# Kernel optimization log

Measured on AMD Instinct MI355X. Metric: run time of the kernel, lower is better.

The kernel has to match this reference:

```python
import jax, jax.numpy as jnp
import numpy as np

VN, BN, NSW, EC, MN = 64, 200, 10, 63, 73
FIN, HID = 32, 64
VLOW, VUPP = 0.9, 1.1


def _ln(z, eps=1e-5):
    m = jnp.mean(z, axis=-1, keepdims=True)
    v = jnp.var(z, axis=-1, keepdims=True)
    return (z - m) * jax.lax.rsqrt(v + eps)


def _layer(x, s, conn, deg_inv, Ws, Wi, Wj, U, Vw, first):
    # dense gated edge update over (B,V,V,H)
    e = jnp.einsum('bvwh,hk->bvwk', s, Ws) + (x @ Wi)[:, :, None, :] + (x @ Wj)[:, None, :, :]
    e = jax.nn.relu(_ln(e))
    s_out = e if first else s + e
    gate = jax.nn.sigmoid(s_out) * conn[None, :, :, None]
    msg = jnp.einsum('bvwh,bwh->bvh', gate, x @ Vw) * deg_inv[None, :, None]  # mean agg
    h = jax.nn.relu(_ln(x @ U + msg))
    return (h if first else x + h), s_out


def setup_inputs() -> dict:
    key = jax.random.key(0)
    ks = jax.random.split(key, 24)
    # radial feeder: path graph (line edges) + long-range tie switches, i<j (triu)
    ea = np.stack([np.arange(VN - 1), np.arange(1, VN)]).astype(np.int32)
    es = np.stack([np.arange(NSW), np.arange(NSW) + 32]).astype(np.int32)
    A = np.zeros((VN, VN), np.float32); A[ea[0], ea[1]] = 1; A[ea[1], ea[0]] = 1
    S = np.zeros((VN, VN), np.float32); S[es[0], es[1]] = 1; S[es[1], es[0]] = 1
    par = np.concatenate([ea[0], es[0]]); chi = np.concatenate([ea[1], es[1]])
    Incp = np.zeros((VN, MN), np.float32); Incp[par, np.arange(MN)] = 1
    Incc = np.zeros((VN, MN), np.float32); Incc[chi, np.arange(MN)] = 1
    deg = (A + S).sum(1)
    Dinv = np.diag((1.0 / np.maximum(deg, 1.0)).astype(np.float32))

    def w(k, shape):
        return jax.random.normal(k, shape, jnp.float32) / np.sqrt(shape[-2])

    return {
        'x': jax.random.normal(ks[0], (BN, VN, FIN), jnp.float32),
        'A': jnp.asarray(A), 'S': jnp.asarray(S),
        'embed_s': jax.random.normal(ks[1], (2, FIN), jnp.float32),
        'p0_Ws': w(ks[2], (FIN, HID)), 'p0_Wi': w(ks[3], (FIN, HID)),
        'p0_Wj': w(ks[4], (FIN, HID)), 'p0_U': w(ks[5], (FIN, HID)),
        'p0_V': w(ks[6], (FIN, HID)),
        'pl_Ws': w(ks[7], (2, HID, HID)), 'pl_Wi': w(ks[8], (2, HID, HID)),
        'pl_Wj': w(ks[9], (2, HID, HID)), 'pl_U': w(ks[10], (2, HID, HID)),
        'pl_V': w(ks[11], (2, HID, HID)),
        'smlp_W1': w(ks[12], (4 * HID, 4 * HID)), 'smlp_W2': w(ks[13], (4 * HID, 4)),
        'cmlp_W1': w(ks[14], (3 * HID, 3 * HID)), 'cmlp_W2': w(ks[15], (3 * HID, 3)),
        'Dinv': jnp.asarray(Dinv), 'Incp': jnp.asarray(Incp), 'Incc': jnp.asarray(Incc),
        'edge_A': jnp.asarray(ea), 'edge_S': jnp.asarray(es),
    }


def reference(x, A, S, embed_s, p0_Ws, p0_Wi, p0_Wj, p0_U, p0_V,
              pl_Ws, pl_Wi, pl_Wj, pl_U, pl_V,
              smlp_W1, smlp_W2, cmlp_W1, cmlp_W2,
              Dinv, Incp, Incc, edge_A, edge_S):
    B = x.shape[0]
    conn = jnp.clip(A + S, 0.0, 1.0)                       # (V,V) union adjacency
    deg_inv = 1.0 / jnp.maximum(conn.sum(1), 1.0)
    # init_embed_edges over dense S -> (B,V,V,FIN)
    s = jnp.broadcast_to(embed_s[S.astype(jnp.int32)][None], (B, VN, VN, FIN))
    xh, s = _layer(x, s, conn, deg_inv, p0_Ws, p0_Wi, p0_Wj, p0_U, p0_V, True)
    for l in range(pl_Ws.shape[0]):
        xh, s = _layer(xh, s, conn, deg_inv, pl_Ws[l], pl_Wi[l], pl_Wj[l], pl_U[l], pl_V[l], False)
    x_g = xh.sum(1)                                        # (B,H) graph feature

    # -- switch head (gather at triu switch edges, identical across batch) --
    si, sj = edge_S[0], edge_S[1]
    xg_s = jnp.broadcast_to(x_g[:, None, :], (B, si.shape[0], HID))
    smlp_in = jnp.concatenate([s[:, si, sj, :], xh[:, si], xh[:, sj], xg_s], axis=-1)
    smlp_out = jax.nn.sigmoid(jax.nn.relu(smlp_in @ smlp_W1) @ smlp_W2)  # (B,nsw,4)
    topology = smlp_out[..., 0]
    graph_topo = jnp.concatenate([jnp.ones((B, MN - NSW), x.dtype), topology], axis=1)
    ps = smlp_out[..., 1] - 0.5
    vs_p = VLOW * (1 - smlp_out[..., 2]) + VUPP * smlp_out[..., 2]
    vs_c = VLOW * (1 - smlp_out[..., 3]) + VUPP * smlp_out[..., 3]

    # -- connection head (gather at triu line edges) --
    ai, aj = edge_A[0], edge_A[1]
    xg_c = jnp.broadcast_to(x_g[:, None, :], (B, ai.shape[0], HID))
    cmlp_in = jnp.concatenate([xh[:, ai], xh[:, aj], xg_c], axis=-1)
    cmlp_out = jax.nn.sigmoid(jax.nn.relu(cmlp_in @ cmlp_W1) @ cmlp_W2)  # (B,Ec,3)
    pc = cmlp_out[..., 0] - 0.5
    vc_p = VLOW * (1 - cmlp_out[..., 1]) + VUPP * cmlp_out[..., 1]
    vc_c = VLOW * (1 - cmlp_out[..., 2]) + VUPP * cmlp_out[..., 2]

    # scatter into (B,M) physics tensors: first M-nsw cols from CMLP, last nsw from SMLP
    p_flow = jnp.concatenate([pc, ps], axis=1)
    v_par = jnp.concatenate([vc_p, vs_p], axis=1)
    v_chi = jnp.concatenate([vc_c, vs_c], axis=1)
    v = v_par @ (Dinv @ Incp).T + v_chi @ (Dinv @ Incc).T   # (B,V)
    v = v.at[:, 0].set(1.0)
    return jnp.concatenate([p_flow, v, graph_topo], axis=1)  # (B, M+V+M)
```

## Files before the change

### kernel.cpp

```cpp
#include <hip/hip_runtime.h>

#define BN 200
#define VN 64
#define HIDD 64
#define FINN 32
#define NSW 10
#define EC 63
#define MNE 73
#define NEDGE 146
#define NPACK 128

typedef unsigned short u16;
typedef unsigned int u32;
typedef __attribute__((ext_vector_type(8))) short bf16x8;
typedef __attribute__((ext_vector_type(4))) float f32x4;

__device__ __forceinline__ float bfu(u16 u) { return __uint_as_float(((u32)u) << 16); }
__device__ __forceinline__ u16 f2bf(float f) {
    u32 x = __float_as_uint(f);
    u32 r = x + 0x7fffu + ((x >> 16) & 1u);
    return (u16)(r >> 16);
}
__device__ __forceinline__ float cvtv(const void* p, int i, int fl) {
    return fl ? bfu(((const u16*)p)[i]) : ((const float*)p)[i];
}

__device__ __forceinline__ int swz(int row, int col) { return col ^ ((row & 7) << 3); }

__device__ __forceinline__ float ldp(const u16* H, const u16* L, int idx) {
    return bfu(H[idx]) + bfu(L[idx]);
}
__device__ __forceinline__ void stp(u16* H, u16* L, int idx, float f) {
    u16 h = f2bf(f);
    H[idx] = h;
    L[idx] = f2bf(f - bfu(h));
}

__device__ __forceinline__ void ln2(float ea, float eb, float& ra, float& rb) {
    float a1 = ea, a2 = ea * ea, b1 = eb, b2 = eb * eb;
#pragma unroll
    for (int m = 1; m < 64; m <<= 1) {
        a1 += __shfl_xor(a1, m);
        a2 += __shfl_xor(a2, m);
        b1 += __shfl_xor(b1, m);
        b2 += __shfl_xor(b2, m);
    }
    float ma = a1 * 0.015625f, mb = b1 * 0.015625f;
    float va = fmaxf(a2 * 0.015625f - ma * ma, 0.f);
    float vb = fmaxf(b2 * 0.015625f - mb * mb, 0.f);
    ra = fmaxf((ea - ma) * rsqrtf(va + 1e-5f), 0.f);
    rb = fmaxf((eb - mb) * rsqrtf(vb + 1e-5f), 0.f);
}

__device__ __forceinline__ void ln4(float ea, float eb, float ec, float ed,
                                    float& ra, float& rb, float& rc, float& rd) {
    float a1 = ea, a2 = ea * ea, b1 = eb, b2 = eb * eb;
    float c1 = ec, c2 = ec * ec, d1 = ed, d2 = ed * ed;
#pragma unroll
    for (int m = 1; m < 64; m <<= 1) {
        a1 += __shfl_xor(a1, m); a2 += __shfl_xor(a2, m);
        b1 += __shfl_xor(b1, m); b2 += __shfl_xor(b2, m);
        c1 += __shfl_xor(c1, m); c2 += __shfl_xor(c2, m);
        d1 += __shfl_xor(d1, m); d2 += __shfl_xor(d2, m);
    }
    float ma = a1 * 0.015625f, mb = b1 * 0.015625f;
    float mc = c1 * 0.015625f, md = d1 * 0.015625f;
    float va = fmaxf(a2 * 0.015625f - ma * ma, 0.f);
    float vb = fmaxf(b2 * 0.015625f - mb * mb, 0.f);
    float vc = fmaxf(c2 * 0.015625f - mc * mc, 0.f);
    float vd = fmaxf(d2 * 0.015625f - md * md, 0.f);
    ra = fmaxf((ea - ma) * rsqrtf(va + 1e-5f), 0.f);
    rb = fmaxf((eb - mb) * rsqrtf(vb + 1e-5f), 0.f);
    rc = fmaxf((ec - mc) * rsqrtf(vc + 1e-5f), 0.f);
    rd = fmaxf((ed - md) * rsqrtf(vd + 1e-5f), 0.f);
}

struct CvtArgs { const void* src[21]; };

__global__ __launch_bounds__(256) void k_prep(CvtArgs ca, const int* __restrict__ eA,
                                              const int* __restrict__ eS,
                                              u16* __restrict__ c1h, u16* __restrict__ c1l,
                                              u16* __restrict__ c2h, u16* __restrict__ c2l,
                                              u16* __restrict__ s1h, u16* __restrict__ s1l,
                                              u16* __restrict__ s2h, u16* __restrict__ s2l,
                                              u16* __restrict__ w0h, u16* __restrict__ w0l,
                                              u16* __restrict__ wlh, u16* __restrict__ wll,
                                              float* __restrict__ ews, float* __restrict__ dinv,
                                              int* __restrict__ row_ptr, int* __restrict__ colp,
                                              int* __restrict__ sw_eidx,
                                              float* __restrict__ dinvD, int* __restrict__ incCnt,
                                              int* __restrict__ incM) {
    int t = threadIdx.x;
    int fl = (((const u16*)ca.src[1])[1] == 0x3F80) ? 1 : 0;
    if (blockIdx.x == 0) {
        __shared__ unsigned char flagL[64 * 65];
        __shared__ float wsL[FINN * 64];
        __shared__ float emL[64];
        __shared__ int degL[64], rpS[65], colS[NEDGE + 16];
        __shared__ int eAL[2 * EC], eSL[2 * NSW];

        if (t < 2 * EC) eAL[t] = eA[t];
        if (t >= 128 && t < 128 + 2 * NSW) eSL[t - 128] = eS[t - 128];
        if (t >= 160 && t < 224) emL[t - 160] = cvtv(ca.src[3], t - 160, fl);
        for (int i = t; i < FINN * 64; i += 256) wsL[i] = cvtv(ca.src[4], i, fl);
        for (int i = t; i < 4096; i += 256) {
            float a = cvtv(ca.src[1], i, fl);
            float s = cvtv(ca.src[2], i, fl);
            int r = i >> 6, c = i & 63;
            flagL[r * 65 + c] = (unsigned char)(((a != 0.f || s != 0.f) ? 1 : 0) |
                                                ((s != 0.f) ? 2 : 0));
        }
        __syncthreads();

        if (t < 128) {
            int j = t >> 6, k = t & 63;
            float a = 0.f;
#pragma unroll
            for (int h = 0; h < FINN; h++) a += emL[j * FINN + h] * wsL[h * 64 + k];
            ews[(j << 6) + k] = a;
        }
        if (t < 64) {
            int d = 0;
#pragma unroll
            for (int w = 0; w < 64; w++) d += flagL[t * 65 + w] & 1;
            degL[t] = d;
            dinv[t] = 1.f / fmaxf((float)d, 1.f);
        }
        __syncthreads();
        if (t == 0) {
            int c = 0;
            for (int v = 0; v < 64; v++) { rpS[v] = c; c += degL[v]; }
            rpS[64] = c;
        }
        __syncthreads();
        if (t < 65) row_ptr[t] = rpS[t];
        if (t < 64) {
            int pos = rpS[t];
#pragma unroll
            for (int w = 0; w < 64; w++) {
                int f = flagL[t * 65 + w];
                if (f & 1) colS[pos++] = w | ((f & 2) ? 256 : 0) | (t << 16);
            }
        }
        __syncthreads();
        int tot = rpS[64];
        if (t < tot) colp[t] = colS[t];
        if (t < NSW) {
            int si = eSL[t], sj = eSL[NSW + t];
            int idx = 0;
            for (int e = rpS[si]; e < rpS[si + 1]; e++)
                if ((colS[e] & 255) == sj) idx = e;
            sw_eidx[t] = idx;
        }
        if (t < 64) {
            dinvD[t] = cvtv(ca.src[18], t * 64 + t, fl);
            int cnt = 0;
            for (int m = 0; m < MNE; m++) {
                int par = (m < EC) ? eAL[m] : eSL[m - EC];
                int chi = (m < EC) ? eAL[EC + m] : eSL[NSW + (m - EC)];
                if (par == t && cnt < 8) incM[t * 8 + cnt++] = (m << 1);
                if (chi == t && cnt < 8) incM[t * 8 + cnt++] = (m << 1) | 1;
            }
            incCnt[t] = cnt;
        }
    } else {
        const int T1 = 36864, T2 = T1 + 3072, T3 = T2 + 65536, T4 = T3 + 4096;
        const int T5 = T4 + 8192, TOT = T5 + 40960;
        for (int i = (blockIdx.x - 1) * 256 + t; i < TOT; i += NPACK * 256) {
            int idx = i;
            const void* src;
            u16 *dh, *dl;
            int K2, N2, nt, rem, loff = 0;
            if (idx < T1) {
                nt = idx / 3072; rem = idx - nt * 3072; src = ca.src[16];
                dh = c1h + idx; dl = c1l + idx; K2 = 192; N2 = 192;
            } else if (idx < T2) {
                idx -= T1; nt = 0; rem = idx; src = ca.src[17];
                dh = c2h + idx; dl = c2l + idx; K2 = 192; N2 = 3;
            } else if (idx < T3) {
                idx -= T2; nt = idx >> 12; rem = idx & 4095; src = ca.src[14];
                dh = s1h + idx; dl = s1l + idx; K2 = 256; N2 = 256;
            } else if (idx < T4) {
                idx -= T3; nt = 0; rem = idx; src = ca.src[15];
                dh = s2h + idx; dl = s2l + idx; K2 = 256; N2 = 4;
            } else if (idx < T5) {
                int j = idx - T4;
                int mt = j >> 11;
                int m2 = j & 2047;
                nt = m2 >> 9; rem = m2 & 511; src = ca.src[5 + mt];
                dh = w0h + j; dl = w0l + j; K2 = 32; N2 = 64;
            } else {
                int j = idx - T5;
                int l = j / 20480;
                int jj = j - l * 20480;
                int mt = jj >> 12;
                int m2 = jj & 4095;
                nt = m2 >> 10; rem = m2 & 1023; src = ca.src[9 + mt];
                loff = l * 4096;
                dh = wlh + j; dl = wll + j; K2 = 64; N2 = 64;
            }
            int kb = rem >> 9, r8 = rem & 511, ln = r8 >> 3, jq = r8 & 7;
            int k = kb * 32 + ((ln >> 4) << 3) + jq;
            int n = nt * 16 + (ln & 15);
            float val = 0.f;
            if (n < N2 && k < K2) val = cvtv(src, loff + k * N2 + n, fl);
            u16 h = f2bf(val);
            *dh = h;
            *dl = f2bf(val - bfu(h));
        }
    }
}

#define XI 0
#define XJ 1
#define XU 2
#define XV 3

__global__ __launch_bounds__(1024) void k_main(
    const void* __restrict__ xraw, const u16* __restrict__ A_u16,
    const int* __restrict__ eA, const int* __restrict__ eS,
    const float* __restrict__ ews, const float* __restrict__ dinv,
    const int* __restrict__ row_ptr, const int* __restrict__ colp,
    const int* __restrict__ sw_eidx,
    const float* __restrict__ dinvD, const int* __restrict__ incCnt, const int* __restrict__ incM,
    const u16* __restrict__ w0h, const u16* __restrict__ w0l,
    const u16* __restrict__ wlh, const u16* __restrict__ wll,
    const u16* __restrict__ c1h, const u16* __restrict__ c1l,
    const u16* __restrict__ c2h, const u16* __restrict__ c2l,
    const u16* __restrict__ s1h, const u16* __restrict__ s1l,
    const u16* __restrict__ s2h, const u16* __restrict__ s2l,
    void* __restrict__ out_v)
{
    __shared__ __align__(16) u16 xHp[64 * 64], xLp[64 * 64];
    __shared__ __align__(16) u16 sHp[NEDGE * 64], sLp[NEDGE * 64];
    __shared__ __align__(16) float preL[NEDGE * 64];
    __shared__ __align__(16) float tLs[4 * 64 * 64];
    __shared__ __align__(16) u16 xgH[64], xgLo[64];
    __shared__ float ewsL[128];
    __shared__ float dinvL[64];
    __shared__ int rpL[65];
    __shared__ int colL[NEDGE + 6];
    __shared__ int swLx[NSW];
    __shared__ int eALs[2 * EC], eSLs[2 * NSW];
    __shared__ float cmoL[EC * 3], smoL[NSW * 4];

    int b = blockIdx.x, t = threadIdx.x;
    int lane = t & 63, wid = t >> 6;
    int m = lane & 15, quad = lane >> 4;
    int fl = (A_u16[1] == 0x3F80) ? 1 : 0;

    for (int i = t; i < 2048; i += 1024) {
        int r = i >> 5, c = i & 31;
        stp(xHp, xLp, (r << 6) + swz(r, c), cvtv(xraw, b * 2048 + i, fl));
    }
    if (t < 128) ewsL[t] = ews[t];
    if (t < 64) dinvL[t] = dinv[t];
    if (t < 65) rpL[t] = row_ptr[t];
    if (t < NEDGE) colL[t] = colp[t];
    if (t < NSW) swLx[t] = sw_eidx[t];
    if (t >= 256 && t < 256 + 2 * EC) eALs[t - 256] = eA[t - 256];
    if (t >= 512 && t < 512 + 2 * NSW) eSLs[t - 512] = eS[t - 512];
    __syncthreads();

    {
        int mat = wid >> 2, Mt = wid & 3;
        const u16* bhp = w0h + mat * 2048;
        const u16* blp = w0l + mat * 2048;
        int row = Mt * 16 + m;
        int c0 = quad * 8;
        bf16x8 ah = *(const bf16x8*)&xHp[(row << 6) + swz(row, c0)];
        bf16x8 al = *(const bf16x8*)&xLp[(row << 6) + swz(row, c0)];
        f32x4 acc[4];
#pragma unroll
        for (int nt = 0; nt < 4; nt++) acc[nt] = (f32x4){0.f, 0.f, 0.f, 0.f};
#pragma unroll
        for (int nt = 0; nt < 4; nt++) {
            int o = (nt << 9) + (lane << 3);
            bf16x8 bh = *(const bf16x8*)(bhp + o);
            bf16x8 bl = *(const bf16x8*)(blp + o);
            acc[nt] = __builtin_amdgcn_mfma_f32_16x16x32_bf16(ah, bh, acc[nt], 0, 0, 0);
            acc[nt] = __builtin_amdgcn_mfma_f32_16x16x32_bf16(al, bh, acc[nt], 0, 0, 0);
            acc[nt] = __builtin_amdgcn_mfma_f32_16x16x32_bf16(ah, bl, acc[nt], 0, 0, 0);
        }
#pragma unroll
        for (int nt = 0; nt < 4; nt++)
#pragma unroll
            for (int r = 0; r < 4; r++) {
                int orow = Mt * 16 + quad * 4 + r;
                tLs[mat * 4096 + (orow << 6) + swz(orow, nt * 16 + m)] = acc[nt][r];
            }
    }
    __syncthreads();

    for (int e = wid; e < NEDGE; e += 32) {
        int e2i = e + 16;
        int has2 = (e2i < NEDGE);
        int eb2 = has2 ? e2i : e;
        int cpa = colL[e], cpb = colL[eb2];
        int wa = cpa & 255, va = (cpa >> 16) & 255;
        int wb = cpb & 255, vb = (cpb >> 16) & 255;
        int sia = (e << 6) + swz(e, lane);
        int sib = (eb2 << 6) + swz(eb2, lane);
        float eea = ewsL[(((cpa >> 8) & 1) << 6) + lane]
                  + tLs[XI * 4096 + (va << 6) + swz(va, lane)]
                  + tLs[XJ * 4096 + (wa << 6) + swz(wa, lane)];
        float eeb = ewsL[(((cpb >> 8) & 1) << 6) + lane]
                  + tLs[XI * 4096 + (vb << 6) + swz(vb, lane)]
                  + tLs[XJ * 4096 + (wb << 6) + swz(wb, lane)];
        float ha, hb;
        ln2(eea, eeb, ha, hb);
        stp(sHp, sLp, sia, ha);
        preL[sia] = tLs[XV * 4096 + (wa << 6) + swz(wa, lane)]
                  * __fdividef(1.f, 1.f + __expf(-ha));
        if (has2) {
            stp(sHp, sLp, sib, hb);
            preL[sib] = tLs[XV * 4096 + (wb << 6) + swz(wb, lane)]
                      * __fdividef(1.f, 1.f + __expf(-hb));
        }
    }
    __syncthreads();

    {
        int v0 = wid << 2;
        float mc0 = 0.f, mc1 = 0.f, mc2 = 0.f, mc3 = 0.f;
        for (int e = rpL[v0]; e < rpL[v0 + 1]; e++) mc0 += preL[(e << 6) + swz(e, lane)];
        for (int e = rpL[v0 + 1]; e < rpL[v0 + 2]; e++) mc1 += preL[(e << 6) + swz(e, lane)];
        for (int e = rpL[v0 + 2]; e < rpL[v0 + 3]; e++) mc2 += preL[(e << 6) + swz(e, lane)];
        for (int e = rpL[v0 + 3]; e < rpL[v0 + 4]; e++) mc3 += preL[(e << 6) + swz(e, lane)];
        float z0 = tLs[XU * 4096 + ((v0 + 0) << 6) + swz(v0 + 0, lane)] + mc0 * dinvL[v0 + 0];
        float z1 = tLs[XU * 4096 + ((v0 + 1) << 6) + swz(v0 + 1, lane)] + mc1 * dinvL[v0 + 1];
        float z2 = tLs[XU * 4096 + ((v0 + 2) << 6) + swz(v0 + 2, lane)] + mc2 * dinvL[v0 + 2];
        float z3 = tLs[XU * 4096 + ((v0 + 3) << 6) + swz(v0 + 3, lane)] + mc3 * dinvL[v0 + 3];
        float h0, h1, h2, h3;
        ln4(z0, z1, z2, z3, h0, h1, h2, h3);
        stp(xHp, xLp, ((v0 + 0) << 6) + swz(v0 + 0, lane), h0);
        stp(xHp, xLp, ((v0 + 1) << 6) + swz(v0 + 1, lane), h1);
        stp(xHp, xLp, ((v0 + 2) << 6) + swz(v0 + 2, lane), h2);
        stp(xHp, xLp, ((v0 + 3) << 6) + swz(v0 + 3, lane), h3);
    }
    __syncthreads();

    for (int l = 0; l < 2; l++) {
        {
            int mat = wid >> 2, Mt = wid & 3;
            const u16* bhp = wlh + l * 20480 + (mat + 1) * 4096;
            const u16* blp = wll + l * 20480 + (mat + 1) * 4096;
            int row = Mt * 16 + m;
            f32x4 acc[4];
#pragma unroll
            for (int nt = 0; nt < 4; nt++) acc[nt] = (f32x4){0.f, 0.f, 0.f, 0.f};
#pragma unroll
            for (int kb = 0; kb < 2; kb++) {
                int c0 = kb * 32 + quad * 8;
                bf16x8 ah = *(const bf16x8*)&xHp[(row << 6) + swz(row, c0)];
                bf16x8 al = *(const bf16x8*)&xLp[(row << 6) + swz(row, c0)];
#pragma unroll
                for (int nt = 0; nt < 4; nt++) {
                    int o = (((nt << 1) + kb) << 9) + (lane << 3);
                    bf16x8 bh = *(const bf16x8*)(bhp + o);
                    bf16x8 bl = *(const bf16x8*)(blp + o);
                    acc[nt] = __builtin_amdgcn_mfma_f32_16x16x32_bf16(ah, bh, acc[nt], 0, 0, 0);
                    acc[nt] = __builtin_amdgcn_mfma_f32_16x16x32_bf16(al, bh, acc[nt], 0, 0, 0);
                    acc[nt] = __builtin_amdgcn_mfma_f32_16x16x32_bf16(ah, bl, acc[nt], 0, 0, 0);
                }
            }
#pragma unroll
            for (int nt = 0; nt < 4; nt++)
#pragma unroll
                for (int r = 0; r < 4; r++) {
                    int orow = Mt * 16 + quad * 4 + r;
                    tLs[mat * 4096 + (orow << 6) + swz(orow, nt * 16 + m)] = acc[nt][r];
                }

            const u16* sbh = wlh + l * 20480;
            const u16* sbl = wll + l * 20480;
            for (int u = wid; u < 40; u += 16) {
                int rt = u >> 2, ntq = u & 3;
                int srow = rt * 16 + m;
                int ar = (srow > NEDGE - 1) ? (NEDGE - 1) : srow;
                f32x4 sacc = (f32x4){0.f, 0.f, 0.f, 0.f};
#pragma unroll
                for (int kb = 0; kb < 2; kb++) {
                    int c0 = kb * 32 + quad * 8;
                    bf16x8 ah = *(const bf16x8*)&sHp[(ar << 6) + swz(ar, c0)];
                    bf16x8 al = *(const bf16x8*)&sLp[(ar << 6) + swz(ar, c0)];
                    int o = (((ntq << 1) + kb) << 9) + (lane << 3);
                    bf16x8 bh = *(const bf16x8*)(sbh + o);
                    bf16x8 bl = *(const bf16x8*)(sbl + o);
                    sacc = __builtin_amdgcn_mfma_f32_16x16x32_bf16(ah, bh, sacc, 0, 0, 0);
                    sacc = __builtin_amdgcn_mfma_f32_16x16x32_bf16(al, bh, sacc, 0, 0, 0);
                    sacc = __builtin_amdgcn_mfma_f32_16x16x32_bf16(ah, bl, sacc, 0, 0, 0);
                }
#pragma unroll
                for (int r = 0; r < 4; r++) {
                    int orow = rt * 16 + quad * 4 + r;
                    if (orow < NEDGE)
                        preL[(orow << 6) + swz(orow, ntq * 16 + m)] = sacc[r];
                }
            }
        }
        __syncthreads();

        for (int e = wid; e < NEDGE; e += 32) {
            int e2i = e + 16;
            int has2 = (e2i < NEDGE);
            int eb2 = has2 ? e2i : e;
            int cpa = colL[e], cpb = colL[eb2];
            int wa = cpa & 255, va = (cpa >> 16) & 255;
            int wb = cpb & 255, vb = (cpb >> 16) & 255;
            int sia = (e << 6) + swz(e, lane);
            int sib = (eb2 << 6) + swz(eb2, lane);
            float eea = preL[sia]
                      + tLs[XI * 4096 + (va << 6) + swz(va, lane)]
                      + tLs[XJ * 4096 + (wa << 6) + swz(wa, lane)];
            float eeb = preL[sib]
                      + tLs[XI * 4096 + (vb << 6) + swz(vb, lane)]
                      + tLs[XJ * 4096 + (wb << 6) + swz(wb, lane)];
            float ha, hb;
            ln2(eea, eeb, ha, hb);
            float souta = ldp(sHp, sLp, sia) + ha;
            float soutb = ldp(sHp, sLp, sib) + hb;
            stp(sHp, sLp, sia, souta);
            preL[sia] = tLs[XV * 4096 + (wa << 6) + swz(wa, lane)]
                      * __fdividef(1.f, 1.f + __expf(-souta));
            if (has2) {
                stp(sHp, sLp, sib, soutb);
                preL[sib] = tLs[XV * 4096 + (wb << 6) + swz(wb, lane)]
                          * __fdividef(1.f, 1.f + __expf(-soutb));
            }
        }
        __syncthreads();

        {
            int v0 = wid << 2;
            float mc0 = 0.f, mc1 = 0.f, mc2 = 0.f, mc3 = 0.f;
            for (int e = rpL[v0]; e < rpL[v0 + 1]; e++) mc0 += preL[(e << 6) + swz(e, lane)];
            for (int e = rpL[v0 + 1]; e < rpL[v0 + 2]; e++) mc1 += preL[(e << 6) + swz(e, lane)];
            for (int e = rpL[v0 + 2]; e < rpL[v0 + 3]; e++) mc2 += preL[(e << 6) + swz(e, lane)];
            for (int e = rpL[v0 + 3]; e < rpL[v0 + 4]; e++) mc3 += preL[(e << 6) + swz(e, lane)];
            float z0 = tLs[XU * 4096 + ((v0 + 0) << 6) + swz(v0 + 0, lane)] + mc0 * dinvL[v0 + 0];
            float z1 = tLs[XU * 4096 + ((v0 + 1) << 6) + swz(v0 + 1, lane)] + mc1 * dinvL[v0 + 1];
            float z2 = tLs[XU * 4096 + ((v0 + 2) << 6) + swz(v0 + 2, lane)] + mc2 * dinvL[v0 + 2];
            float z3 = tLs[XU * 4096 + ((v0 + 3) << 6) + swz(v0 + 3, lane)] + mc3 * dinvL[v0 + 3];
            float h0, h1, h2, h3;
            ln4(z0, z1, z2, z3, h0, h1, h2, h3);
            int i0 = ((v0 + 0) << 6) + swz(v0 + 0, lane);
            int i1 = ((v0 + 1) << 6) + swz(v0 + 1, lane);
            int i2 = ((v0 + 2) << 6) + swz(v0 + 2, lane);
            int i3 = ((v0 + 3) << 6) + swz(v0 + 3, lane);
            float x0 = ldp(xHp, xLp, i0) + h0;
            float x1 = ldp(xHp, xLp, i1) + h1;
            float x2 = ldp(xHp, xLp, i2) + h2;
            float x3 = ldp(xHp, xLp, i3) + h3;
            stp(xHp, xLp, i0, x0);
            stp(xHp, xLp, i1, x1);
            stp(xHp, xLp, i2, x2);
            stp(xHp, xLp, i3, x3);
            if (l == 1) tLs[(wid << 6) + lane] = x0 + x1 + x2 + x3;
        }
        __syncthreads();
    }

    if (t < 64) {
        float s = 0.f;
#pragma unroll
        for (int i = 0; i < 16; i++) s += tLs[(i << 6) + t];
        stp(xgH, xgLo, t, s);
    }
    __syncthreads();

    u16* tp  = (u16*)tLs;
    u16* hcH = tp;
    u16* hcL = tp + 12288;
    u16* hsH = tp + 24576;
    u16* hsL = tp + 28672;

    if (wid < 12) {
        int Mt = wid & 3, ntg = wid >> 2;
        int e = Mt * 16 + m; if (e > 62) e = 62;
        int ai = eALs[e], aj = eALs[EC + e];
        f32x4 acc[4];
#pragma unroll
        for (int j = 0; j < 4; j++) acc[j] = (f32x4){0.f, 0.f, 0.f, 0.f};
#pragma unroll
        for (int kb = 0; kb < 6; kb++) {
            int k = kb * 32 + quad * 8;
            bf16x8 ah, al;
            if (k < 64) {
                ah = *(const bf16x8*)&xHp[(ai << 6) + swz(ai, k)];
                al = *(const bf16x8*)&xLp[(ai << 6) + swz(ai, k)];
            } else if (k < 128) {
                int c = k - 64;
                ah = *(const bf16x8*)&xHp[(aj << 6) + swz(aj, c)];
                al = *(const bf16x8*)&xLp[(aj << 6) + swz(aj, c)];
            } else {
                int c = k - 128;
                ah = *(const bf16x8*)&xgH[c];
                al = *(const bf16x8*)&xgLo[c];
            }
#pragma unroll
            for (int j = 0; j < 4; j++) {
                int nt = ntg * 4 + j;
                int o = ((nt * 6 + kb) << 9) + (lane << 3);
                bf16x8 bh = *(const bf16x8*)(c1h + o);
                bf16x8 bl = *(const bf16x8*)(c1l + o);
                acc[j] = __builtin_amdgcn_mfma_f32_16x16x32_bf16(ah, bh, acc[j], 0, 0, 0);
                acc[j] = __builtin_amdgcn_mfma_f32_16x16x32_bf16(al, bh, acc[j], 0, 0, 0);
                acc[j] = __builtin_amdgcn_mfma_f32_16x16x32_bf16(ah, bl, acc[j], 0, 0, 0);
            }
        }
#pragma unroll
        for (int j = 0; j < 4; j++) {
            int nt = ntg * 4 + j;
#pragma unroll
            for (int r = 0; r < 4; r++) {
                int row = Mt * 16 + quad * 4 + r;
                stp(hcH, hcL, row * 192 + swz(row, nt * 16 + m), fmaxf(acc[j][r], 0.f));
            }
        }
    } else {
        int e2 = (m > 9) ? 9 : m;
        int si = eSLs[e2], sj = eSLs[NSW + e2];
        int sw = swLx[e2];
#pragma unroll
        for (int j = 0; j < 4; j++) {
            int nt = (wid - 12) * 4 + j;
            f32x4 accS = (f32x4){0.f, 0.f, 0.f, 0.f};
#pragma unroll
            for (int kb = 0; kb < 8; kb++) {
                int k = kb * 32 + quad * 8;
                bf16x8 ah, al;
                if (k < 64) {
                    ah = *(const bf16x8*)&sHp[(sw << 6) + swz(sw, k)];
                    al = *(const bf16x8*)&sLp[(sw << 6) + swz(sw, k)];
                } else if (k < 128) {
                    int c = k - 64;
                    ah = *(const bf16x8*)&xHp[(si << 6) + swz(si, c)];
                    al = *(const bf16x8*)&xLp[(si << 6) + swz(si, c)];
                } else if (k < 192) {
                    int c = k - 128;
                    ah = *(const bf16x8*)&xHp[(sj << 6) + swz(sj, c)];
                    al = *(const bf16x8*)&xLp[(sj << 6) + swz(sj, c)];
                } else {
                    int c = k - 192;
                    ah = *(const bf16x8*)&xgH[c];
                    al = *(const bf16x8*)&xgLo[c];
                }
                int o = ((nt * 8 + kb) << 9) + (lane << 3);
                bf16x8 bh = *(const bf16x8*)(s1h + o);
                bf16x8 bl = *(const bf16x8*)(s1l + o);
                accS = __builtin_amdgcn_mfma_f32_16x16x32_bf16(ah, bh, accS, 0, 0, 0);
                accS = __builtin_amdgcn_mfma_f32_16x16x32_bf16(al, bh, accS, 0, 0, 0);
                accS = __builtin_amdgcn_mfma_f32_16x16x32_bf16(ah, bl, accS, 0, 0, 0);
            }
#pragma unroll
            for (int r = 0; r < 4; r++) {
                int row = quad * 4 + r;
                stp(hsH, hsL, (row << 8) + swz(row, nt * 16 + m), fmaxf(accS[r], 0.f));
            }
        }
    }
    __syncthreads();

    if (wid < 4) {
        f32x4 accD = (f32x4){0.f, 0.f, 0.f, 0.f};
        int row = wid * 16 + m;
#pragma unroll
        for (int kb = 0; kb < 6; kb++) {
            int c0 = kb * 32 + quad * 8;
            bf16x8 ah = *(const bf16x8*)&hcH[row * 192 + swz(row, c0)];
            bf16x8 al = *(const bf16x8*)&hcL[row * 192 + swz(row, c0)];
            int o = (kb << 9) + (lane << 3);
            bf16x8 bh = *(const bf16x8*)(c2h + o);
            bf16x8 bl = *(const bf16x8*)(c2l + o);
            accD = __builtin_amdgcn_mfma_f32_16x16x32_bf16(ah, bh, accD, 0, 0, 0);
            accD = __builtin_amdgcn_mfma_f32_16x16x32_bf16(al, bh, accD, 0, 0, 0);
            accD = __builtin_amdgcn_mfma_f32_16x16x32_bf16(ah, bl, accD, 0, 0, 0);
        }
#pragma unroll
        for (int r = 0; r < 4; r++) {
            int row2 = wid * 16 + quad * 4 + r;
            if (row2 < EC && m < 3)
                cmoL[row2 * 3 + m] = 1.f / (1.f + __expf(-accD[r]));
        }
    } else if (wid == 4) {
        f32x4 accT = (f32x4){0.f, 0.f, 0.f, 0.f};
#pragma unroll
        for (int kb = 0; kb < 8; kb++) {
            int c0 = kb * 32 + quad * 8;
            bf16x8 ah = *(const bf16x8*)&hsH[(m << 8) + swz(m, c0)];
            bf16x8 al = *(const bf16x8*)&hsL[(m << 8) + swz(m, c0)];
            int o = (kb << 9) + (lane << 3);
            bf16x8 bh = *(const bf16x8*)(s2h + o);
            bf16x8 bl = *(const bf16x8*)(s2l + o);
            accT = __builtin_amdgcn_mfma_f32_16x16x32_bf16(ah, bh, accT, 0, 0, 0);
            accT = __builtin_amdgcn_mfma_f32_16x16x32_bf16(al, bh, accT, 0, 0, 0);
            accT = __builtin_amdgcn_mfma_f32_16x16x32_bf16(ah, bl, accT, 0, 0, 0);
        }
#pragma unroll
        for (int r = 0; r < 4; r++) {
            int row = quad * 4 + r;
            if (row < NSW && m < 4)
                smoL[row * 4 + m] = 1.f / (1.f + __expf(-accT[r]));
        }
    }
    __syncthreads();

    if (t < 2 * MNE + VN) {
        float val;
        if (t < MNE) {
            val = (t < EC) ? cmoL[t * 3] - 0.5f : smoL[(t - EC) * 4 + 1] - 0.5f;
        } else if (t < MNE + VN) {
            int i = t - MNE;
            if (i == 0) {
                val = 1.0f;
            } else {
                float acc = 0.f;
                int c = incCnt[i];
                for (int q = 0; q < c; q++) {
                    int em = incM[i * 8 + q];
                    int mm = em >> 1, role = em & 1;
                    float vv = (mm < EC) ? 0.9f + 0.2f * cmoL[mm * 3 + 1 + role]
                                         : 0.9f + 0.2f * smoL[(mm - EC) * 4 + 2 + role];
                    acc += vv;
                }
                val = acc * dinvD[i];
            }
        } else {
            int mm = t - (MNE + VN);
            val = (mm < EC) ? 1.0f : smoL[(mm - EC) * 4];
        }
        size_t oidx = (size_t)b * (2 * MNE + VN) + t;
        if (fl) ((u16*)out_v)[oidx] = f2bf(val);
        else    ((float*)out_v)[oidx] = val;
    }
}

extern "C" void kernel_launch(void* const* d_in, const int* in_sizes, int n_in,
                              void* d_out, int out_size, void* d_ws, size_t ws_size,
                              hipStream_t stream) {
    const int* eA = (const int*)d_in[21];
    const int* eS = (const int*)d_in[22];

    float* pool = (float*)d_ws;
    float* ews     = pool;
    float* dinv    = ews + 128;
    float* dinvD   = dinv + 64;
    int*   row_ptr = (int*)(dinvD + 64);
    int*   colp    = row_ptr + 80;
    int*   sw_eidx = colp + 256;
    int*   incCnt  = sw_eidx + 16;
    int*   incM    = incCnt + 64;
    u16*   c1h = (u16*)(incM + 512);
    u16*   c1l = c1h + 36864;
    u16*   c2h = c1l + 36864;
    u16*   c2l = c2h + 3072;
    u16*   s1h = c2l + 3072;
    u16*   s1l = s1h + 65536;
    u16*   s2h = s1l + 65536;
    u16*   s2l = s2h + 4096;
    u16*   w0h = s2l + 4096;
    u16*   w0l = w0h + 8192;
    u16*   wlh = w0l + 8192;
    u16*   wll = wlh + 40960;

    CvtArgs ca;
    for (int i = 0; i < 21; i++) ca.src[i] = d_in[i];

    k_prep<<<1 + NPACK, 256, 0, stream>>>(ca, eA, eS,
                                          c1h, c1l, c2h, c2l, s1h, s1l, s2h, s2l,
                                          w0h, w0l, wlh, wll,
                                          ews, dinv, row_ptr, colp, sw_eidx,
                                          dinvD, incCnt, incM);

    k_main<<<BN, 1024, 0, stream>>>(d_in[0], (const u16*)d_in[1], eA, eS,
                                    ews, dinv, row_ptr, colp, sw_eidx,
                                    dinvD, incCnt, incM,
                                    w0h, w0l, wlh, wll,
                                    c1h, c1l, c2h, c2l, s1h, s1l, s2h, s2l,
                                    d_out);
}
```

Before: 179.7 us.

## Pack hi/lo bf16 pairs into u32 LDS words, use DPP layer-norm reductions

Interleaves the high and low bf16 halves of each split-precision value into one 32-bit LDS word, so scalar loads and stores touch one array and the MFMA fragments are rebuilt from two 128-bit loads with bit shuffles. The swizzle is changed to match the new word granularity. Layer-norm reductions switch from xor-shuffle butterflies to DPP row operations plus readlane. The switch-head GEMM loop is reordered so each A fragment is loaded once and reused across four output tiles. This trades fewer LDS transactions and shuffles for extra ALU unpacking work and higher register pressure.

```diff
diff --git a/kernel.cpp b/kernel.cpp
--- a/kernel.cpp
+++ b/kernel.cpp
@@ -14,6 +14,7 @@
 typedef unsigned int u32;
 typedef __attribute__((ext_vector_type(8))) short bf16x8;
 typedef __attribute__((ext_vector_type(4))) float f32x4;
+typedef __attribute__((ext_vector_type(4))) u32 u32x4;
 
 __device__ __forceinline__ float bfu(u16 u) { return __uint_as_float(((u32)u) << 16); }
 __device__ __forceinline__ u16 f2bf(float f) {
@@ -25,54 +26,54 @@
     return fl ? bfu(((const u16*)p)[i]) : ((const float*)p)[i];
 }
 
-__device__ __forceinline__ int swz(int row, int col) { return col ^ ((row & 7) << 3); }
-
-__device__ __forceinline__ float ldp(const u16* H, const u16* L, int idx) {
-    return bfu(H[idx]) + bfu(L[idx]);
-}
-__device__ __forceinline__ void stp(u16* H, u16* L, int idx, float f) {
+__device__ __forceinline__ int swzp(int row, int col) { return col ^ ((row & 7) << 2); }
+
+__device__ __forceinline__ float ldp1(const u32* P, int idx) {
+    u32 v = P[idx];
+    return __uint_as_float(v << 16) + __uint_as_float(v & 0xffff0000u);
+}
+__device__ __forceinline__ void stp1(u32* P, int idx, float f) {
     u16 h = f2bf(f);
-    H[idx] = h;
-    L[idx] = f2bf(f - bfu(h));
-}
-
-__device__ __forceinline__ void ln2(float ea, float eb, float& ra, float& rb) {
-    float a1 = ea, a2 = ea * ea, b1 = eb, b2 = eb * eb;
-#pragma unroll
-    for (int m = 1; m < 64; m <<= 1) {
-        a1 += __shfl_xor(a1, m);
-        a2 += __shfl_xor(a2, m);
-        b1 += __shfl_xor(b1, m);
-        b2 += __shfl_xor(b2, m);
-    }
-    float ma = a1 * 0.015625f, mb = b1 * 0.015625f;
-    float va = fmaxf(a2 * 0.015625f - ma * ma, 0.f);
-    float vb = fmaxf(b2 * 0.015625f - mb * mb, 0.f);
-    ra = fmaxf((ea - ma) * rsqrtf(va + 1e-5f), 0.f);
-    rb = fmaxf((eb - mb) * rsqrtf(vb + 1e-5f), 0.f);
-}
-
-__device__ __forceinline__ void ln4(float ea, float eb, float ec, float ed,
-                                    float& ra, float& rb, float& rc, float& rd) {
-    float a1 = ea, a2 = ea * ea, b1 = eb, b2 = eb * eb;
-    float c1 = ec, c2 = ec * ec, d1 = ed, d2 = ed * ed;
-#pragma unroll
-    for (int m = 1; m < 64; m <<= 1) {
-        a1 += __shfl_xor(a1, m); a2 += __shfl_xor(a2, m);
-        b1 += __shfl_xor(b1, m); b2 += __shfl_xor(b2, m);
-        c1 += __shfl_xor(c1, m); c2 += __shfl_xor(c2, m);
-        d1 += __shfl_xor(d1, m); d2 += __shfl_xor(d2, m);
-    }
-    float ma = a1 * 0.015625f, mb = b1 * 0.015625f;
-    float mc = c1 * 0.015625f, md = d1 * 0.015625f;
-    float va = fmaxf(a2 * 0.015625f - ma * ma, 0.f);
-    float vb = fmaxf(b2 * 0.015625f - mb * mb, 0.f);
-    float vc = fmaxf(c2 * 0.015625f - mc * mc, 0.f);
-    float vd = fmaxf(d2 * 0.015625f - md * md, 0.f);
-    ra = fmaxf((ea - ma) * rsqrtf(va + 1e-5f), 0.f);
-    rb = fmaxf((eb - mb) * rsqrtf(vb + 1e-5f), 0.f);
-    rc = fmaxf((ec - mc) * rsqrtf(vc + 1e-5f), 0.f);
-    rd = fmaxf((ed - md) * rsqrtf(vd + 1e-5f), 0.f);
+    u16 l = f2bf(f - bfu(h));
+    P[idx] = (u32)h | ((u32)l << 16);
+}
+
+__device__ __forceinline__ void ldfrag(const u32* P, int i0, int i1, bf16x8* ah, bf16x8* al) {
+    u32x4 w0 = *(const u32x4*)&P[i0];
+    u32x4 w1 = *(const u32x4*)&P[i1];
+    union { bf16x8 v; u32 w[4]; } A, L;
+    A.w[0] = (w0.x & 0xffffu) | (w0.y << 16);
+    A.w[1] = (w0.z & 0xffffu) | (w0.w << 16);
+    A.w[2] = (w1.x & 0xffffu) | (w1.y << 16);
+    A.w[3] = (w1.z & 0xffffu) | (w1.w << 16);
+    L.w[0] = (w0.x >> 16) | (w0.y & 0xffff0000u);
+    L.w[1] = (w0.z >> 16) | (w0.w & 0xffff0000u);
+    L.w[2] = (w1.x >> 16) | (w1.y & 0xffff0000u);
+    L.w[3] = (w1.z >> 16) | (w1.w & 0xffff0000u);
+    *ah = A.v;
+    *al = L.v;
+}
+
+template <int CTRL>
+__device__ __forceinline__ float dppadd(float x) {
+    int v = __builtin_amdgcn_update_dpp(0, __float_as_int(x), CTRL, 0xf, 0xf, 1);
+    return x + __int_as_float(v);
+}
+__device__ __forceinline__ float wtot64(float x) {
+    x = dppadd<0x111>(x);
+    x = dppadd<0x112>(x);
+    x = dppadd<0x114>(x);
+    x = dppadd<0x118>(x);
+    x = dppadd<0x142>(x);
+    x = dppadd<0x143>(x);
+    return __int_as_float(__builtin_amdgcn_readlane(__float_as_int(x), 63));
+}
+__device__ __forceinline__ float ln_dpp(float e) {
+    float s1 = wtot64(e);
+    float s2 = wtot64(e * e);
+    float mean = s1 * 0.015625f;
+    float var = fmaxf(s2 * 0.015625f - mean * mean, 0.f);
+    return fmaxf((e - mean) * rsqrtf(var + 1e-5f), 0.f);
 }
 
 struct CvtArgs { const void* src[21]; };
@@ -231,11 +232,11 @@
     const u16* __restrict__ s2h, const u16* __restrict__ s2l,
     void* __restrict__ out_v)
 {
-    __shared__ __align__(16) u16 xHp[64 * 64], xLp[64 * 64];
-    __shared__ __align__(16) u16 sHp[NEDGE * 64], sLp[NEDGE * 64];
+    __shared__ __align__(16) u32 xP[64 * 64];
+    __shared__ __align__(16) u32 sP[NEDGE * 64];
     __shared__ __align__(16) float preL[NEDGE * 64];
     __shared__ __align__(16) float tLs[4 * 64 * 64];
-    __shared__ __align__(16) u16 xgH[64], xgLo[64];
+    __shared__ __align__(16) u32 xgPk[64];
     __shared__ float ewsL[128];
     __shared__ float dinvL[64];
     __shared__ int rpL[65];
@@ -251,7 +252,7 @@
 
     for (int i = t; i < 2048; i += 1024) {
         int r = i >> 5, c = i & 31;
-        stp(xHp, xLp, (r << 6) + swz(r, c), cvtv(xraw, b * 2048 + i, fl));
+        stp1(xP, (r << 6) + swzp(r, c), cvtv(xraw, b * 2048 + i, fl));
     }
     if (t < 128) ewsL[t] = ews[t];
     if (t < 64) dinvL[t] = dinv[t];
@@ -268,8 +269,8 @@
         const u16* blp = w0l + mat * 2048;
         int row = Mt * 16 + m;
         int c0 = quad * 8;
-        bf16x8 ah = *(const bf16x8*)&xHp[(row << 6) + swz(row, c0)];
-        bf16x8 al = *(const bf16x8*)&xLp[(row << 6) + swz(row, c0)];
+        bf16x8 ah, al;
+        ldfrag(xP, (row << 6) + swzp(row, c0), (row << 6) + swzp(row, c0 + 4), &ah, &al);
         f32x4 acc[4];
 #pragma unroll
         for (int nt = 0; nt < 4; nt++) acc[nt] = (f32x4){0.f, 0.f, 0.f, 0.f};
@@ -287,7 +288,7 @@
 #pragma unroll
             for (int r = 0; r < 4; r++) {
                 int orow = Mt * 16 + quad * 4 + r;
-                tLs[mat * 4096 + (orow << 6) + swz(orow, nt * 16 + m)] = acc[nt][r];
+                tLs[mat * 4096 + (orow << 6) + swzp(orow, nt * 16 + m)] = acc[nt][r];
             }
     }
     __syncthreads();
@@ -299,22 +300,22 @@
         int cpa = colL[e], cpb = colL[eb2];
         int wa = cpa & 255, va = (cpa >> 16) & 255;
         int wb = cpb & 255, vb = (cpb >> 16) & 255;
-        int sia = (e << 6) + swz(e, lane);
-        int sib = (eb2 << 6) + swz(eb2, lane);
+        int sia = (e << 6) + swzp(e, lane);
+        int sib = (eb2 << 6) + swzp(eb2, lane);
         float eea = ewsL[(((cpa >> 8) & 1) << 6) + lane]
-                  + tLs[XI * 4096 + (va << 6) + swz(va, lane)]
-                  + tLs[XJ * 4096 + (wa << 6) + swz(wa, lane)];
+                  + tLs[XI * 4096 + (va << 6) + swzp(va, lane)]
+                  + tLs[XJ * 4096 + (wa << 6) + swzp(wa, lane)];
         float eeb = ewsL[(((cpb >> 8) & 1) << 6) + lane]
-                  + tLs[XI * 4096 + (vb << 6) + swz(vb, lane)]
-                  + tLs[XJ * 4096 + (wb << 6) + swz(wb, lane)];
-        float ha, hb;
-        ln2(eea, eeb, ha, hb);
-        stp(sHp, sLp, sia, ha);
-        preL[sia] = tLs[XV * 4096 + (wa << 6) + swz(wa, lane)]
+                  + tLs[XI * 4096 + (vb << 6) + swzp(vb, lane)]
+                  + tLs[XJ * 4096 + (wb << 6) + swzp(wb, lane)];
+        float ha = ln_dpp(eea);
+        float hb = ln_dpp(eeb);
+        stp1(sP, sia, ha);
+        preL[sia] = tLs[XV * 4096 + (wa << 6) + swzp(wa, lane)]
                   * __fdividef(1.f, 1.f + __expf(-ha));
         if (has2) {
-            stp(sHp, sLp, sib, hb);
-            preL[sib] = tLs[XV * 4096 + (wb << 6) + swz(wb, lane)]
+            stp1(sP, sib, hb);
+            preL[sib] = tLs[XV * 4096 + (wb << 6) + swzp(wb, lane)]
                       * __fdividef(1.f, 1.f + __expf(-hb));
         }
     }
@@ -323,20 +324,19 @@
     {
         int v0 = wid << 2;
         float mc0 = 0.f, mc1 = 0.f, mc2 = 0.f, mc3 = 0.f;
-        for (int e = rpL[v0]; e < rpL[v0 + 1]; e++) mc0 += preL[(e << 6) + swz(e, lane)];
-        for (int e = rpL[v0 + 1]; e < rpL[v0 + 2]; e++) mc1 += preL[(e << 6) + swz(e, lane)];
-        for (int e = rpL[v0 + 2]; e < rpL[v0 + 3]; e++) mc2 += preL[(e << 6) + swz(e, lane)];
-        for (int e = rpL[v0 + 3]; e < rpL[v0 + 4]; e++) mc3 += preL[(e << 6) + swz(e, lane)];
-        float z0 = tLs[XU * 4096 + ((v0 + 0) << 6) + swz(v0 + 0, lane)] + mc0 * dinvL[v0 + 0];
-        float z1 = tLs[XU * 4096 + ((v0 + 1) << 6) + swz(v0 + 1, lane)] + mc1 * dinvL[v0 + 1];
-        float z2 = tLs[XU * 4096 + ((v0 + 2) << 6) + swz(v0 + 2, lane)] + mc2 * dinvL[v0 + 2];
-        float z3 = tLs[XU * 4096 + ((v0 + 3) << 6) + swz(v0 + 3, lane)] + mc3 * dinvL[v0 + 3];
-        float h0, h1, h2, h3;
-        ln4(z0, z1, z2, z3, h0, h1, h2, h3);
-        stp(xHp, xLp, ((v0 + 0) << 6) + swz(v0 + 0, lane), h0);
-        stp(xHp, xLp, ((v0 + 1) << 6) + swz(v0 + 1, lane), h1);
-        stp(xHp, xLp, ((v0 + 2) << 6) + swz(v0 + 2, lane), h2);
-        stp(xHp, xLp, ((v0 + 3) << 6) + swz(v0 + 3, lane), h3);
+        for (int e = rpL[v0]; e < rpL[v0 + 1]; e++) mc0 += preL[(e << 6) + swzp(e, lane)];
+        for (int e = rpL[v0 + 1]; e < rpL[v0 + 2]; e++) mc1 += preL[(e << 6) + swzp(e, lane)];
+        for (int e = rpL[v0 + 2]; e < rpL[v0 + 3]; e++) mc2 += preL[(e << 6) + swzp(e, lane)];
+        for (int e = rpL[v0 + 3]; e < rpL[v0 + 4]; e++) mc3 += preL[(e << 6) + swzp(e, lane)];
+        float z0 = tLs[XU * 4096 + ((v0 + 0) << 6) + swzp(v0 + 0, lane)] + mc0 * dinvL[v0 + 0];
+        float z1 = tLs[XU * 4096 + ((v0 + 1) << 6) + swzp(v0 + 1, lane)] + mc1 * dinvL[v0 + 1];
+        float z2 = tLs[XU * 4096 + ((v0 + 2) << 6) + swzp(v0 + 2, lane)] + mc2 * dinvL[v0 + 2];
+        float z3 = tLs[XU * 4096 + ((v0 + 3) << 6) + swzp(v0 + 3, lane)] + mc3 * dinvL[v0 + 3];
+        float h0 = ln_dpp(z0), h1 = ln_dpp(z1), h2 = ln_dpp(z2), h3 = ln_dpp(z3);
+        stp1(xP, ((v0 + 0) << 6) + swzp(v0 + 0, lane), h0);
+        stp1(xP, ((v0 + 1) << 6) + swzp(v0 + 1, lane), h1);
+        stp1(xP, ((v0 + 2) << 6) + swzp(v0 + 2, lane), h2);
+        stp1(xP, ((v0 + 3) << 6) + swzp(v0 + 3, lane), h3);
     }
     __syncthreads();
 
@@ -352,8 +352,8 @@
 #pragma unroll
             for (int kb = 0; kb < 2; kb++) {
                 int c0 = kb * 32 + quad * 8;
-                bf16x8 ah = *(const bf16x8*)&xHp[(row << 6) + swz(row, c0)];
-                bf16x8 al = *(const bf16x8*)&xLp[(row << 6) + swz(row, c0)];
+                bf16x8 ah, al;
+                ldfrag(xP, (row << 6) + swzp(row, c0), (row << 6) + swzp(row, c0 + 4), &ah, &al);
 #pragma unroll
                 for (int nt = 0; nt < 4; nt++) {
                     int o = (((nt << 1) + kb) << 9) + (lane << 3);
@@ -369,7 +369,7 @@
 #pragma unroll
                 for (int r = 0; r < 4; r++) {
                     int orow = Mt * 16 + quad * 4 + r;
-                    tLs[mat * 4096 + (orow << 6) + swz(orow, nt * 16 + m)] = acc[nt][r];
+                    tLs[mat * 4096 + (orow << 6) + swzp(orow, nt * 16 + m)] = acc[nt][r];
                 }
 
             const u16* sbh = wlh + l * 20480;
@@ -382,8 +382,8 @@
 #pragma unroll
                 for (int kb = 0; kb < 2; kb++) {
                     int c0 = kb * 32 + quad * 8;
-                    bf16x8 ah = *(const bf16x8*)&sHp[(ar << 6) + swz(ar, c0)];
-                    bf16x8 al = *(const bf16x8*)&sLp[(ar << 6) + swz(ar, c0)];
+                    bf16x8 ah, al;
+                    ldfrag(sP, (ar << 6) + swzp(ar, c0), (ar << 6) + swzp(ar, c0 + 4), &ah, &al);
                     int o = (((ntq << 1) + kb) << 9) + (lane << 3);
                     bf16x8 bh = *(const bf16x8*)(sbh + o);
                     bf16x8 bl = *(const bf16x8*)(sbl + o);
@@ -395,7 +395,7 @@
                 for (int r = 0; r < 4; r++) {
                     int orow = rt * 16 + quad * 4 + r;
                     if (orow < NEDGE)
-                        preL[(orow << 6) + swz(orow, ntq * 16 + m)] = sacc[r];
+                        preL[(orow << 6) + swzp(orow, ntq * 16 + m)] = sacc[r];
                 }
             }
         }
@@ -408,24 +408,24 @@
             int cpa = colL[e], cpb = colL[eb2];
             int wa = cpa & 255, va = (cpa >> 16) & 255;
             int wb = cpb & 255, vb = (cpb >> 16) & 255;
-            int sia = (e << 6) + swz(e, lane);
-            int sib = (eb2 << 6) + swz(eb2, lane);
+            int sia = (e << 6) + swzp(e, lane);
+            int sib = (eb2 << 6) + swzp(eb2, lane);
             float eea = preL[sia]
-                      + tLs[XI * 4096 + (va << 6) + swz(va, lane)]
-                      + tLs[XJ * 4096 + (wa << 6) + swz(wa, lane)];
+                      + tLs[XI * 4096 + (va << 6) + swzp(va, lane)]
+                      + tLs[XJ * 4096 + (wa << 6) + swzp(wa, lane)];
             float eeb = preL[sib]
-                      + tLs[XI * 4096 + (vb << 6) + swz(vb, lane)]
-                      + tLs[XJ * 4096 + (wb << 6) + swz(wb, lane)];
-            float ha, hb;
-            ln2(eea, eeb, ha, hb);
-            float souta = ldp(sHp, sLp, sia) + ha;
-            float soutb = ldp(sHp, sLp, sib) + hb;
-            stp(sHp, sLp, sia, souta);
-            preL[sia] = tLs[XV * 4096 + (wa << 6) + swz(wa, lane)]
+                      + tLs[XI * 4096 + (vb << 6) + swzp(vb, lane)]
+                      + tLs[XJ * 4096 + (wb << 6) + swzp(wb, lane)];
+            float ha = ln_dpp(eea);
+            float hb = ln_dpp(eeb);
+            float souta = ldp1(sP, sia) + ha;
+            float soutb = ldp1(sP, sib) + hb;
+            stp1(sP, sia, souta);
+            preL[sia] = tLs[XV * 4096 + (wa << 6) + swzp(wa, lane)]
                       * __fdividef(1.f, 1.f + __expf(-souta));
             if (has2) {
-                stp(sHp, sLp, sib, soutb);
-                preL[sib] = tLs[XV * 4096 + (wb << 6) + swz(wb, lane)]
+                stp1(sP, sib, soutb);
+                preL[sib] = tLs[XV * 4096 + (wb << 6) + swzp(wb, lane)]
                           * __fdividef(1.f, 1.f + __expf(-soutb));
             }
         }
@@ -434,28 +434,27 @@
         {
             int v0 = wid << 2;
             float mc0 = 0.f, mc1 = 0.f, mc2 = 0.f, mc3 = 0.f;
-            for (int e = rpL[v0]; e < rpL[v0 + 1]; e++) mc0 += preL[(e << 6) + swz(e, lane)];
-            for (int e = rpL[v0 + 1]; e < rpL[v0 + 2]; e++) mc1 += preL[(e << 6) + swz(e, lane)];
-            for (int e = rpL[v0 + 2]; e < rpL[v0 + 3]; e++) mc2 += preL[(e << 6) + swz(e, lane)];
-            for (int e = rpL[v0 + 3]; e < rpL[v0 + 4]; e++) mc3 += preL[(e << 6) + swz(e, lane)];
-            float z0 = tLs[XU * 4096 + ((v0 + 0) << 6) + swz(v0 + 0, lane)] + mc0 * dinvL[v0 + 0];
-            float z1 = tLs[XU * 4096 + ((v0 + 1) << 6) + swz(v0 + 1, lane)] + mc1 * dinvL[v0 + 1];
-            float z2 = tLs[XU * 4096 + ((v0 + 2) << 6) + swz(v0 + 2, lane)] + mc2 * dinvL[v0 + 2];
-            float z3 = tLs[XU * 4096 + ((v0 + 3) << 6) + swz(v0 + 3, lane)] + mc3 * dinvL[v0 + 3];
-            float h0, h1, h2, h3;
-            ln4(z0, z1, z2, z3, h0, h1, h2, h3);
-            int i0 = ((v0 + 0) << 6) + swz(v0 + 0, lane);
-            int i1 = ((v0 + 1) << 6) + swz(v0 + 1, lane);
-            int i2 = ((v0 + 2) << 6) + swz(v0 + 2, lane);
-            int i3 = ((v0 + 3) << 6) + swz(v0 + 3, lane);
-            float x0 = ldp(xHp, xLp, i0) + h0;
-            float x1 = ldp(xHp, xLp, i1) + h1;
-            float x2 = ldp(xHp, xLp, i2) + h2;
-            float x3 = ldp(xHp, xLp, i3) + h3;
-            stp(xHp, xLp, i0, x0);
-            stp(xHp, xLp, i1, x1);
-            stp(xHp, xLp, i2, x2);
-            stp(xHp, xLp, i3, x3);
+            for (int e = rpL[v0]; e < rpL[v0 + 1]; e++) mc0 += preL[(e << 6) + swzp(e, lane)];
+            for (int e = rpL[v0 + 1]; e < rpL[v0 + 2]; e++) mc1 += preL[(e << 6) + swzp(e, lane)];
+            for (int e = rpL[v0 + 2]; e < rpL[v0 + 3]; e++) mc2 += preL[(e << 6) + swzp(e, lane)];
+            for (int e = rpL[v0 + 3]; e < rpL[v0 + 4]; e++) mc3 += preL[(e << 6) + swzp(e, lane)];
+            float z0 = tLs[XU * 4096 + ((v0 + 0) << 6) + swzp(v0 + 0, lane)] + mc0 * dinvL[v0 + 0];
+            float z1 = tLs[XU * 4096 + ((v0 + 1) << 6) + swzp(v0 + 1, lane)] + mc1 * dinvL[v0 + 1];
+            float z2 = tLs[XU * 4096 + ((v0 + 2) << 6) + swzp(v0 + 2, lane)] + mc2 * dinvL[v0 + 2];
+            float z3 = tLs[XU * 4096 + ((v0 + 3) << 6) + swzp(v0 + 3, lane)] + mc3 * dinvL[v0 + 3];
+            float h0 = ln_dpp(z0), h1 = ln_dpp(z1), h2 = ln_dpp(z2), h3 = ln_dpp(z3);
+            int i0 = ((v0 + 0) << 6) + swzp(v0 + 0, lane);
+            int i1 = ((v0 + 1) << 6) + swzp(v0 + 1, lane);
+            int i2 = ((v0 + 2) << 6) + swzp(v0 + 2, lane);
+            int i3 = ((v0 + 3) << 6) + swzp(v0 + 3, lane);
+            float x0 = ldp1(xP, i0) + h0;
+            float x1 = ldp1(xP, i1) + h1;
+            float x2 = ldp1(xP, i2) + h2;
+            float x3 = ldp1(xP, i3) + h3;
+            stp1(xP, i0, x0);
+            stp1(xP, i1, x1);
+            stp1(xP, i2, x2);
+            stp1(xP, i3, x3);
             if (l == 1) tLs[(wid << 6) + lane] = x0 + x1 + x2 + x3;
         }
         __syncthreads();
@@ -465,15 +464,12 @@
         float s = 0.f;
 #pragma unroll
         for (int i = 0; i < 16; i++) s += tLs[(i << 6) + t];
-        stp(xgH, xgLo, t, s);
+        stp1(xgPk, t, s);
     }
     __syncthreads();
 
-    u16* tp  = (u16*)tLs;
-    u16* hcH = tp;
-    u16* hcL = tp + 12288;
-    u16* hsH = tp + 24576;
-    u16* hsL = tp + 28672;
+    u32* hcP = (u32*)tLs;
+    u32* hsP = (u32*)tLs + 12288;
 
     if (wid < 12) {
         int Mt = wid & 3, ntg = wid >> 2;
@@ -487,16 +483,13 @@
             int k = kb * 32 + quad * 8;
             bf16x8 ah, al;
             if (k < 64) {
-                ah = *(const bf16x8*)&xHp[(ai << 6) + swz(ai, k)];
-                al = *(const bf16x8*)&xLp[(ai << 6) + swz(ai, k)];
+                ldfrag(xP, (ai << 6) + swzp(ai, k), (ai << 6) + swzp(ai, k + 4), &ah, &al);
             } else if (k < 128) {
                 int c = k - 64;
-                ah = *(const bf16x8*)&xHp[(aj << 6) + swz(aj, c)];
-                al = *(const bf16x8*)&xLp[(aj << 6) + swz(aj, c)];
+                ldfrag(xP, (aj << 6) + swzp(aj, c), (aj << 6) + swzp(aj, c + 4), &ah, &al);
             } else {
                 int c = k - 128;
-                ah = *(const bf16x8*)&xgH[c];
-                al = *(const bf16x8*)&xgLo[c];
+                ldfrag(xgPk, c, c + 4, &ah, &al);
             }
 #pragma unroll
             for (int j = 0; j < 4; j++) {
@@ -515,48 +508,50 @@
 #pragma unroll
             for (int r = 0; r < 4; r++) {
                 int row = Mt * 16 + quad * 4 + r;
-                stp(hcH, hcL, row * 192 + swz(row, nt * 16 + m), fmaxf(acc[j][r], 0.f));
+                stp1(hcP, row * 192 + swzp(row, nt * 16 + m), fmaxf(acc[j][r], 0.f));
             }
         }
     } else {
         int e2 = (m > 9) ? 9 : m;
         int si = eSLs[e2], sj = eSLs[NSW + e2];
         int sw = swLx[e2];
-#pragma unroll
-        for (int j = 0; j < 4; j++) {
-            int nt = (wid - 12) * 4 + j;
-            f32x4 accS = (f32x4){0.f, 0.f, 0.f, 0.f};
-#pragma unroll
-            for (int kb = 0; kb < 8; kb++) {
-                int k = kb * 32 + quad * 8;
-                bf16x8 ah, al;
-                if (k < 64) {
-                    ah = *(const bf16x8*)&sHp[(sw << 6) + swz(sw, k)];
-                    al = *(const bf16x8*)&sLp[(sw << 6) + swz(sw, k)];
-                } else if (k < 128) {
-                    int c = k - 64;
-                    ah = *(const bf16x8*)&xHp[(si << 6) + swz(si, c)];
-                    al = *(const bf16x8*)&xLp[(si << 6) + swz(si, c)];
-                } else if (k < 192) {
-                    int c = k - 128;
-                    ah = *(const bf16x8*)&xHp[(sj << 6) + swz(sj, c)];
-                    al = *(const bf16x8*)&xLp[(sj << 6) + swz(sj, c)];
-                } else {
-                    int c = k - 192;
-                    ah = *(const bf16x8*)&xgH[c];
-                    al = *(const bf16x8*)&xgLo[c];
-                }
+        f32x4 accS[4];
+#pragma unroll
+        for (int j = 0; j < 4; j++) accS[j] = (f32x4){0.f, 0.f, 0.f, 0.f};
+#pragma unroll
+        for (int kb = 0; kb < 8; kb++) {
+            int k = kb * 32 + quad * 8;
+            bf16x8 ah, al;
+            if (k < 64) {
+                ldfrag(sP, (sw << 6) + swzp(sw, k), (sw << 6) + swzp(sw, k + 4), &ah, &al);
+            } else if (k < 128) {
+                int c = k - 64;
+                ldfrag(xP, (si << 6) + swzp(si, c), (si << 6) + swzp(si, c + 4), &ah, &al);
+            } else if (k < 192) {
+                int c = k - 128;
+                ldfrag(xP, (sj << 6) + swzp(sj, c), (sj << 6) + swzp(sj, c + 4), &ah, &al);
+            } else {
+                int c = k - 192;
+                ldfrag(xgPk, c, c + 4, &ah, &al);
+            }
+#pragma unroll
+            for (int j = 0; j < 4; j++) {
+                int nt = (wid - 12) * 4 + j;
                 int o = ((nt * 8 + kb) << 9) + (lane << 3);
                 bf16x8 bh = *(const bf16x8*)(s1h + o);
                 bf16x8 bl = *(const bf16x8*)(s1l + o);
-                accS = __builtin_amdgcn_mfma_f32_16x16x32_bf16(ah, bh, accS, 0, 0, 0);
-                accS = __builtin_amdgcn_mfma_f32_16x16x32_bf16(al, bh, accS, 0, 0, 0);
-                accS = __builtin_amdgcn_mfma_f32_16x16x32_bf16(ah, bl, accS, 0, 0, 0);
-            }
+                accS[j] = __builtin_amdgcn_mfma_f32_16x16x32_bf16(ah, bh, accS[j], 0, 0, 0);
+                accS[j] = __builtin_amdgcn_mfma_f32_16x16x32_bf16(al, bh, accS[j], 0, 0, 0);
+                accS[j] = __builtin_amdgcn_mfma_f32_16x16x32_bf16(ah, bl, accS[j], 0, 0, 0);
+            }
+        }
+#pragma unroll
+        for (int j = 0; j < 4; j++) {
+            int nt = (wid - 12) * 4 + j;
 #pragma unroll
             for (int r = 0; r < 4; r++) {
                 int row = quad * 4 + r;
-                stp(hsH, hsL, (row << 8) + swz(row, nt * 16 + m), fmaxf(accS[r], 0.f));
+                stp1(hsP, (row << 8) + swzp(row, nt * 16 + m), fmaxf(accS[j][r], 0.f));
             }
         }
     }
@@ -568,8 +563,8 @@
 #pragma unroll
         for (int kb = 0; kb < 6; kb++) {
             int c0 = kb * 32 + quad * 8;
-            bf16x8 ah = *(const bf16x8*)&hcH[row * 192 + swz(row, c0)];
-            bf16x8 al = *(const bf16x8*)&hcL[row * 192 + swz(row, c0)];
+            bf16x8 ah, al;
+            ldfrag(hcP, row * 192 + swzp(row, c0), row * 192 + swzp(row, c0 + 4), &ah, &al);
             int o = (kb << 9) + (lane << 3);
             bf16x8 bh = *(const bf16x8*)(c2h + o);
             bf16x8 bl = *(const bf16x8*)(c2l + o);
@@ -588,8 +583,8 @@
 #pragma unroll
         for (int kb = 0; kb < 8; kb++) {
             int c0 = kb * 32 + quad * 8;
-            bf16x8 ah = *(const bf16x8*)&hsH[(m << 8) + swz(m, c0)];
-            bf16x8 al = *(const bf16x8*)&hsL[(m << 8) + swz(m, c0)];
+            bf16x8 ah, al;
+            ldfrag(hsP, (m << 8) + swzp(m, c0), (m << 8) + swzp(m, c0 + 4), &ah, &al);
             int o = (kb << 9) + (lane << 3);
             bf16x8 bh = *(const bf16x8*)(s2h + o);
             bf16x8 bl = *(const bf16x8*)(s2l + o);
```

New measurement: 169.1 us. 5.9% less time.
